# Kernel optimization log

Hardware: AMD Instinct MI355X
Metric: run time of the kernel (lower is better)

Reference implementation:

```python
import jax, jax.numpy as jnp
import numpy as np

B, L, V, D, H = 4096, 32, 50000, 300, 6
HD = D // H  # 50


def setup_inputs() -> dict:
    key = jax.random.key(0)
    ks = jax.random.split(key, 9)
    s = 0.02
    return {
        "title": jax.random.randint(ks[0], (B, L), 0, V),
        "emb": jax.random.normal(ks[1], (V, D), dtype=jnp.float32) * s,
        "pos_emb": jax.random.normal(ks[2], (512, D), dtype=jnp.float32) * s,
        "Wq": jax.random.normal(ks[3], (D, D), dtype=jnp.float32) * s,
        "bq": jnp.zeros((D,), jnp.float32),
        "Wk": jax.random.normal(ks[4], (D, D), dtype=jnp.float32) * s,
        "bk": jnp.zeros((D,), jnp.float32),
        "Wv": jax.random.normal(ks[5], (D, D), dtype=jnp.float32) * s,
        "bv": jnp.zeros((D,), jnp.float32),
        "Wo": jax.random.normal(ks[6], (D, D), dtype=jnp.float32) * s,
        "bo": jnp.zeros((D,), jnp.float32),
        "Va": jax.random.normal(ks[7], (D, D), dtype=jnp.float32) * s,
        "ba": jnp.zeros((D,), jnp.float32),
        "qw": jax.random.normal(ks[8], (D, 1), dtype=jnp.float32) * s,
    }


def reference(title, emb, pos_emb, Wq, bq, Wk, bk, Wv, bv, Wo, bo, Va, ba, qw):
    b, l = title.shape
    # word embedding + positional embedding
    x = emb[title] + pos_emb[:l][None, :, :]  # [B, L, D]

    def heads(y):  # [B, L, D] -> [B, H, L, HD]
        return y.reshape(b, l, H, HD).transpose(0, 2, 1, 3)

    # manual multi-head self-attention (mask is all-ones -> no masking effect)
    q = heads(x @ Wq.T + bq) / jnp.sqrt(jnp.float32(HD))
    k = heads(x @ Wk.T + bk)
    v = heads(x @ Wv.T + bv)
    scores = jnp.einsum("bhqd,bhkd->bhqk", q, k)  # [B, H, L, L]
    w = jax.nn.softmax(scores, axis=-1)  # dropout is identity in eval
    ctx = jnp.einsum("bhqk,bhkd->bhqd", w, v)
    ctx = ctx.transpose(0, 2, 1, 3).reshape(b, l, D)
    ctx = ctx @ Wo.T + bo  # [B, L, D]

    # additive attention pooling
    t = jnp.tanh(ctx @ Va.T + ba)          # [B, L, D]
    a = (t @ qw)[..., 0]                    # [B, L]
    alpha = jax.nn.softmax(a, axis=1)       # [B, L]
    out = jnp.einsum("bs,bsd->bd", alpha, ctx)  # [B, D]
    return out
```

## Files before the change

kernel.cpp:

```cpp
#include <hip/hip_runtime.h>
#include <math.h>

typedef _Float16 f16;
typedef _Float16 half8 __attribute__((ext_vector_type(8)));
typedef _Float16 half4 __attribute__((ext_vector_type(4)));
typedef float float4v __attribute__((ext_vector_type(4)));
typedef int int4v __attribute__((ext_vector_type(4)));

#define MFMA16(a, b, c) __builtin_amdgcn_mfma_f32_16x16x32_f16((a), (b), (c), 0, 0, 0)


#define WQKV_OFF 0u
#define BQKV_OFF 655360u
#define WO_OFF   659456u
#define WVA_OFF  864256u
#define BVA_OFF  1069056u
#define CBAR_OFF 1070336u
#define XF_OFF   3691776u

__device__ __forceinline__ float fast_tanh(float x) {
    float e = __expf(2.f * x);
    return 1.f - 2.f / (e + 1.f);
}

__global__ void repack1(const float* __restrict__ Wq, const float* __restrict__ Wk,
                        const float* __restrict__ Wv, const float* __restrict__ Wo,
                        const float* __restrict__ bq, const float* __restrict__ bk,
                        const float* __restrict__ bv,
                        f16* __restrict__ wqkvF, f16* __restrict__ wo16F,
                        float* __restrict__ bqkv) {
    int idx = blockIdx.x * 256 + threadIdx.x;
    const float rs = 0.14142135623730951f;
    if (idx < 327680) {
        int ntile = idx / 5120, rem = idx - ntile * 5120;
        int ks = rem / 512, r2 = rem - ks * 512;
        int lane = r2 >> 3, j = r2 & 7;
        int n = ntile * 16 + (lane & 15);
        int k = ks * 32 + (lane >> 4) * 8 + j;
        int g = n / 320, r = n - g * 320;
        float v = 0.f;
        if (r < 300 && k < 300) {
            if (g == 0) v = Wq[r * 300 + k] * rs;
            else if (g == 1) v = Wk[r * 300 + k];
            else if (g == 2) v = Wv[r * 300 + k];
        }
        wqkvF[idx] = (f16)v;
    } else if (idx < 430080) {
        int t = idx - 327680;
        int ntile = t / 5120, rem = t - ntile * 5120;
        int ks = rem / 512, r2 = rem - ks * 512;
        int lane = r2 >> 3, j = r2 & 7;
        int n = ntile * 16 + (lane & 15);
        int k = ks * 32 + (lane >> 4) * 8 + j;
        wo16F[t] = (f16)((n < 300 && k < 300) ? Wo[n * 300 + k] : 0.f);
    } else if (idx < 431104) {
        int n = idx - 430080;
        int g = n / 320, r = n - g * 320;
        float v = 0.f;
        if (r < 300) {
            if (g == 0) v = bq[r] * rs;
            else if (g == 1) v = bk[r];
            else if (g == 2) v = bv[r];
        }
        bqkv[n] = v;
    }
}

__global__ void repack2(const float* __restrict__ Va, const float* __restrict__ Wo,
                        f16* __restrict__ wvaF) {
    int bt = blockIdx.x;
    int mt = bt / 20, nt = bt % 20;
    int lane = threadIdx.x & 63;
    int lr = lane & 15, quad = lane >> 4;
    float4v acc = {0.f, 0.f, 0.f, 0.f};
    int m = mt * 16 + lr;
    int nn = nt * 16 + lr;
    for (int ks = 0; ks < 10; ++ks) {
        int c = ks * 32 + quad * 8;
        half8 af, bf;
#pragma unroll
        for (int j = 0; j < 8; ++j) {
            int cc = c + j;
            af[j] = (f16)((m < 300 && cc < 300) ? Va[m * 300 + cc] : 0.f);
            bf[j] = (f16)((nn < 300 && cc < 300) ? Wo[cc * 300 + nn] : 0.f);
        }
        acc = MFMA16(af, bf, acc);
    }
#pragma unroll
    for (int r = 0; r < 4; ++r) {
        int row = mt * 16 + quad * 4 + r;
        int col = nt * 16 + lr;
        int addr = ((row >> 4) * 10 + (col >> 5)) * 512 +
                   (((col >> 3) & 3) * 16 + (row & 15)) * 8 + (col & 7);
        wvaF[addr] = (f16)acc[r];
    }
}

__global__ void repack3(const float* __restrict__ Va, const float* __restrict__ bo,
                        const float* __restrict__ ba, float* __restrict__ bva) {
    int j = threadIdx.x;
    float s = 0.f;
    if (j < 300) {
        for (int k = 0; k < 300; ++k) s += Va[j * 300 + k] * bo[k];
        s += ba[j];
    }
    bva[j] = s;
}

__global__ void gather_kernel(const int* __restrict__ title, const float* __restrict__ emb,
                              const float* __restrict__ pos, f16* __restrict__ xF) {
    int c = blockIdx.x * 256 + threadIdx.x;
    int fragblk = c >> 6, lane = c & 63;
    int item = fragblk / 20, rem = fragblk - item * 20;
    int mt = rem / 10, ks = rem - mt * 10;
    int lr = lane & 15, quad = lane >> 4;
    int row = item * 32 + mt * 16 + lr;
    int col = ks * 32 + quad * 8;
    int t = title[row];
    int l = row & 31;
    half8 h;
    if (col + 8 <= 300) {
        float4v e0 = *(const float4v*)&emb[t * 300 + col];
        float4v e1 = *(const float4v*)&emb[t * 300 + col + 4];
        float4v p0 = *(const float4v*)&pos[l * 300 + col];
        float4v p1 = *(const float4v*)&pos[l * 300 + col + 4];
#pragma unroll
        for (int j = 0; j < 4; ++j) { h[j] = (f16)(e0[j] + p0[j]); h[4 + j] = (f16)(e1[j] + p1[j]); }
    } else {
#pragma unroll
        for (int j = 0; j < 8; ++j) {
            int cc = col + j;
            h[j] = (f16)((cc < 300) ? emb[t * 300 + cc] + pos[l * 300 + cc] : 0.f);
        }
    }
    *(half8*)&xF[c * 8] = h;
}

__global__ __launch_bounds__(512, 4) void qkvattn_kernel(
    const f16* __restrict__ xF, const f16* __restrict__ wqkvF,
    const float* __restrict__ bqkv, const f16* __restrict__ wvaF,
    const float* __restrict__ bva, const float* __restrict__ qw,
    f16* __restrict__ cbar) {
    __shared__ __align__(16) f16 qL[6 * 32 * 72];
    __shared__ __align__(16) f16 kL[6 * 32 * 72];
    __shared__ __align__(16) f16 vT[6 * 64 * 32];
    __shared__ float aL[32];
    const int ib = blockIdx.x, tid = threadIdx.x;
    const int w = tid >> 6, lane = tid & 63, lr = lane & 15, quad = lane >> 4;
    const float4v vz = {0.f, 0.f, 0.f, 0.f};
    const int4v z4 = {0, 0, 0, 0};

    for (int i = tid; i < 1344; i += 512) {
        int hrow = i / 7, c = i - hrow * 7;
        ((int*)&qL[hrow * 72 + 50])[c] = 0;
        ((int*)&kL[hrow * 72 + 50])[c] = 0;
    }
    for (int i = tid; i < 336; i += 512) {
        int t = i >> 2, c4 = i & 3;
        int h = t / 14, d = 50 + (t - (t / 14) * 14);
        ((int4v*)&vT[(h * 64 + d) * 32])[c4] = z4;
    }
    if (tid < 32) aL[tid] = 0.f;

    {
        float bb[8];
#pragma unroll
        for (int j = 0; j < 8; ++j) bb[j] = bqkv[(w * 8 + j) * 16 + lr];
        float4v acc[2][8];
#pragma unroll
        for (int mt = 0; mt < 2; ++mt)
#pragma unroll
            for (int j = 0; j < 8; ++j) acc[mt][j] = vz;
#pragma unroll
        for (int ks = 0; ks < 10; ++ks) {
            half8 a0 = *(const half8*)&xF[(((ib * 2 + 0) * 10 + ks) * 64 + lane) * 8];
            half8 a1 = *(const half8*)&xF[(((ib * 2 + 1) * 10 + ks) * 64 + lane) * 8];
#pragma unroll
            for (int j = 0; j < 8; ++j) {
                int tile = w * 8 + j;
                if (tile < 60) {
                    half8 bf = *(const half8*)&wqkvF[((tile * 10 + ks) * 64 + lane) * 8];
                    acc[0][j] = MFMA16(a0, bf, acc[0][j]);
                    acc[1][j] = MFMA16(a1, bf, acc[1][j]);
                }
            }
        }
#pragma unroll
        for (int j = 0; j < 8; ++j) {
            int tile = w * 8 + j;
            int wi = tile / 20;
            int n = tile * 16 + lr;
            int cc = n - wi * 320;
            if (wi < 3 && cc < 300) {
                int h = cc / 50, d = cc - h * 50;
                if (wi == 2) {
#pragma unroll
                    for (int mt = 0; mt < 2; ++mt) {
                        int row0 = mt * 16 + quad * 4;
                        half4 pk;
#pragma unroll
                        for (int r = 0; r < 4; ++r) pk[r] = (f16)(acc[mt][j][r] + bb[j]);
                        int idx = (h * 64 + d) * 32 + row0;
                        int byt = (idx * 2) ^ (((d >> 2) & 3) << 4);
                        *(half4*)((char*)vT + byt) = pk;
                    }
                } else {
                    f16* dst = (wi == 0) ? qL : kL;
#pragma unroll
                    for (int mt = 0; mt < 2; ++mt)
#pragma unroll
                        for (int r = 0; r < 4; ++r) {
                            int row = mt * 16 + quad * 4 + r;
                            dst[(h * 32 + row) * 72 + d] = (f16)(acc[mt][j][r] + bb[j]);
                        }
                }
            }
        }
    }
    __syncthreads();

    const int hh = w;
    if (w < 6) {
        float4v s00 = vz, s01 = vz, s10 = vz, s11 = vz;
#pragma unroll
        for (int ks = 0; ks < 2; ++ks) {
            int c = ks * 32 + quad * 8;
            half8 aq0 = *(const half8*)&qL[(hh * 32 + lr) * 72 + c];
            half8 aq1 = *(const half8*)&qL[(hh * 32 + 16 + lr) * 72 + c];
            half8 bk0 = *(const half8*)&kL[(hh * 32 + lr) * 72 + c];
            half8 bk1 = *(const half8*)&kL[(hh * 32 + 16 + lr) * 72 + c];
            s00 = MFMA16(aq0, bk0, s00);
            s01 = MFMA16(aq0, bk1, s01);
            s10 = MFMA16(aq1, bk0, s10);
            s11 = MFMA16(aq1, bk1, s11);
        }
        f16* ph = qL + hh * 32 * 72;
#pragma unroll
        for (int mt = 0; mt < 2; ++mt) {
            float4v sv0 = mt ? s10 : s00;
            float4v sv1 = mt ? s11 : s01;
#pragma unroll
            for (int r = 0; r < 4; ++r) {
                float v0 = sv0[r], v1 = sv1[r];
                float m = fmaxf(v0, v1);
#pragma unroll
                for (int off = 1; off < 16; off <<= 1) m = fmaxf(m, __shfl_xor(m, off, 64));
                float e0 = __expf(v0 - m), e1 = __expf(v1 - m);
                float ss = e0 + e1;
#pragma unroll
                for (int off = 1; off < 16; off <<= 1) ss += __shfl_xor(ss, off, 64);
                float inv = 1.0f / ss;
                int row = mt * 16 + quad * 4 + r;
                ph[row * 40 + lr] = (f16)(e0 * inv);
                ph[row * 40 + 16 + lr] = (f16)(e1 * inv);
            }
        }
    }
    __syncthreads();

    f16* scratch = kL;
    for (int i = tid; i < 32 * 28; i += 512) {
        int row = i / 28, cc = 300 + (i - row * 28);
        scratch[row * 328 + cc] = (f16)0.f;
    }
    if (w < 6) {
        int h = hh;
        f16* ph = qL + hh * 32 * 72;
        half8 aw0 = *(const half8*)&ph[lr * 40 + quad * 8];
        half8 aw1 = *(const half8*)&ph[(16 + lr) * 40 + quad * 8];
        float4v c0[4], c1[4];
#pragma unroll
        for (int nt = 0; nt < 4; ++nt) { c0[nt] = vz; c1[nt] = vz; }
#pragma unroll
        for (int nt = 0; nt < 4; ++nt) {
            int rIdx = nt * 16 + lr;
            int idx = (hh * 64 + rIdx) * 32 + quad * 8;
            int byt = (idx * 2) ^ (((rIdx >> 2) & 3) << 4);
            half8 bvf = *(const half8*)((const char*)vT + byt);
            c0[nt] = MFMA16(aw0, bvf, c0[nt]);
            c1[nt] = MFMA16(aw1, bvf, c1[nt]);
        }
#pragma unroll
        for (int mt = 0; mt < 2; ++mt)
#pragma unroll
            for (int nt = 0; nt < 4; ++nt)
#pragma unroll
                for (int r = 0; r < 4; ++r) {
                    int d = nt * 16 + lr;
                    if (d < 50) {
                        int row = mt * 16 + quad * 4 + r;
                        float4v cv = mt ? c1[nt] : c0[nt];
                        scratch[row * 328 + h * 50 + d] = (f16)cv[r];
                    }
                }
    }

    const int mtile = w >> 2, nsub = w & 3;
    half8 pbf[5];
    float pbva[5], pqw[5];
#pragma unroll
    for (int i = 0; i < 5; ++i) {
        int n = (nsub * 5 + i) * 16 + lr;
        pbf[i] = *(const half8*)&wvaF[(((nsub * 5 + i) * 10) * 64 + lane) * 8];
        pbva[i] = bva[n];
        pqw[i] = (n < 300) ? qw[n] : 0.f;
    }
    __syncthreads();

    {
        float4v vacc[5];
#pragma unroll
        for (int i = 0; i < 5; ++i) vacc[i] = vz;
        const int arow = (mtile * 16 + lr) * 328;
        {
            half8 a = *(const half8*)&scratch[arow + quad * 8];
#pragma unroll
            for (int i = 0; i < 5; ++i) vacc[i] = MFMA16(a, pbf[i], vacc[i]);
        }
#pragma unroll
        for (int ks = 1; ks < 10; ++ks) {
            half8 a = *(const half8*)&scratch[arow + ks * 32 + quad * 8];
#pragma unroll
            for (int i = 0; i < 5; ++i) {
                half8 bf = *(const half8*)&wvaF[((((nsub * 5 + i) * 10) + ks) * 64 + lane) * 8];
                vacc[i] = MFMA16(a, bf, vacc[i]);
            }
        }
        float ps[4] = {0.f, 0.f, 0.f, 0.f};
#pragma unroll
        for (int i = 0; i < 5; ++i) {
#pragma unroll
            for (int r = 0; r < 4; ++r) ps[r] += fast_tanh(vacc[i][r] + pbva[i]) * pqw[i];
        }
#pragma unroll
        for (int r = 0; r < 4; ++r)
#pragma unroll
            for (int off = 1; off < 16; off <<= 1) ps[r] += __shfl_xor(ps[r], off, 64);
        if (lr == 0) {
#pragma unroll
            for (int r = 0; r < 4; ++r) atomicAdd(&aL[mtile * 16 + quad * 4 + r], ps[r]);
        }
    }
    __syncthreads();

    {
        float av = aL[lane & 31];
        float m5 = av;
#pragma unroll
        for (int off = 1; off < 32; off <<= 1) m5 = fmaxf(m5, __shfl_xor(m5, off, 32));
        float e5 = __expf(av - m5);
        float ss5 = e5;
#pragma unroll
        for (int off = 1; off < 32; off <<= 1) ss5 += __shfl_xor(ss5, off, 32);
        float al = e5 / ss5;
        if (tid < 320) {
            int d = tid;
            float acc = 0.f;
#pragma unroll
            for (int l = 0; l < 32; ++l)
                acc += __shfl(al, l, 32) * (float)scratch[l * 328 + d];
            cbar[ib * 320 + d] = (f16)acc;
        }
    }
}

__global__ __launch_bounds__(512) void out_kernel(
    const f16* __restrict__ cbar, const f16* __restrict__ wo16F,
    const float* __restrict__ bo, float* __restrict__ out) {
    __shared__ __align__(16) f16 cA[32 * 328];
    const int mb = blockIdx.x, tid = threadIdx.x;
    const int w = tid >> 6, lane = tid & 63, lr = lane & 15, quad = lane >> 4;
    const int mh = w >> 2, nsub = w & 3;
    for (int i = tid; i < 1280; i += 512) {
        int row = i / 40, g = i - row * 40;
        *(half8*)&cA[row * 328 + g * 8] = *(const half8*)&cbar[(mb * 32 + row) * 320 + g * 8];
    }
    __syncthreads();
    const float4v vz = {0.f, 0.f, 0.f, 0.f};
    float4v acc[5];
#pragma unroll
    for (int i = 0; i < 5; ++i) acc[i] = vz;
#pragma unroll
    for (int ks = 0; ks < 10; ++ks) {
        half8 a = *(const half8*)&cA[(mh * 16 + lr) * 328 + ks * 32 + quad * 8];
#pragma unroll
        for (int i = 0; i < 5; ++i) {
            half8 bf = *(const half8*)&wo16F[((((nsub * 5 + i) * 10) + ks) * 64 + lane) * 8];
            acc[i] = MFMA16(a, bf, acc[i]);
        }
    }
#pragma unroll
    for (int i = 0; i < 5; ++i) {
        int n = (nsub * 5 + i) * 16 + lr;
        if (n < 300) {
            float bb = bo[n];
#pragma unroll
            for (int r = 0; r < 4; ++r)
                out[(mb * 32 + mh * 16 + quad * 4 + r) * 300 + n] = acc[i][r] + bb;
        }
    }
}

extern "C" void kernel_launch(void* const* d_in, const int* in_sizes, int n_in,
                              void* d_out, int out_size, void* d_ws, size_t ws_size,
                              hipStream_t stream) {
    const int* title = (const int*)d_in[0];
    const float* emb = (const float*)d_in[1];
    const float* pos = (const float*)d_in[2];
    const float* Wq = (const float*)d_in[3];
    const float* bq = (const float*)d_in[4];
    const float* Wk = (const float*)d_in[5];
    const float* bk = (const float*)d_in[6];
    const float* Wv = (const float*)d_in[7];
    const float* bv = (const float*)d_in[8];
    const float* Wo = (const float*)d_in[9];
    const float* bo = (const float*)d_in[10];
    const float* Va = (const float*)d_in[11];
    const float* ba = (const float*)d_in[12];
    const float* qw = (const float*)d_in[13];
    char* ws = (char*)d_ws;
    float* out = (float*)d_out;

    f16* wqkvF = (f16*)(ws + WQKV_OFF);
    float* bqkv = (float*)(ws + BQKV_OFF);
    f16* wo16F = (f16*)(ws + WO_OFF);
    f16* wvaF = (f16*)(ws + WVA_OFF);
    float* bva = (float*)(ws + BVA_OFF);
    f16* cbar = (f16*)(ws + CBAR_OFF);
    f16* xF = (f16*)(ws + XF_OFF);

    repack1<<<1684, 256, 0, stream>>>(Wq, Wk, Wv, Wo, bq, bk, bv, wqkvF, wo16F, bqkv);
    repack2<<<400, 64, 0, stream>>>(Va, Wo, wvaF);
    repack3<<<1, 320, 0, stream>>>(Va, bo, ba, bva);
    gather_kernel<<<20480, 256, 0, stream>>>(title, emb, pos, xF);
    qkvattn_kernel<<<4096, 512, 0, stream>>>(xF, wqkvF, bqkv, wvaF, bva, qw, cbar);
    out_kernel<<<128, 512, 0, stream>>>(cbar, wo16F, bo, out);
}
```

Baseline: 446.4 us.

## Fuse embedding gather into attention kernel and parallelize bias fold

The standalone gather kernel, which wrote the f16 embedding+position fragments to a global buffer, is removed. Each attention block now gathers its own 32 rows straight into shared memory, reusing the vT buffer before V is written, and runs the QKV MFMAs from LDS. This drops a global round trip of the activations and one launch, at the cost of an extra block barrier and exposed gather latency inside the main kernel. The single-block bias precompute is also spread over 320 wavefronts with a shuffle reduction.

```diff
diff --git a/kernel.cpp b/kernel.cpp
--- a/kernel.cpp
+++ b/kernel.cpp
@@ -16,7 +16,6 @@
 #define WVA_OFF  864256u
 #define BVA_OFF  1069056u
 #define CBAR_OFF 1070336u
-#define XF_OFF   3691776u
 
 __device__ __forceinline__ float fast_tanh(float x) {
     float e = __expf(2.f * x);
@@ -98,49 +97,23 @@
 
 __global__ void repack3(const float* __restrict__ Va, const float* __restrict__ bo,
                         const float* __restrict__ ba, float* __restrict__ bva) {
-    int j = threadIdx.x;
+    int j = blockIdx.x;
+    int lane = threadIdx.x;
     float s = 0.f;
     if (j < 300) {
-        for (int k = 0; k < 300; ++k) s += Va[j * 300 + k] * bo[k];
-        s += ba[j];
-    }
-    bva[j] = s;
-}
-
-__global__ void gather_kernel(const int* __restrict__ title, const float* __restrict__ emb,
-                              const float* __restrict__ pos, f16* __restrict__ xF) {
-    int c = blockIdx.x * 256 + threadIdx.x;
-    int fragblk = c >> 6, lane = c & 63;
-    int item = fragblk / 20, rem = fragblk - item * 20;
-    int mt = rem / 10, ks = rem - mt * 10;
-    int lr = lane & 15, quad = lane >> 4;
-    int row = item * 32 + mt * 16 + lr;
-    int col = ks * 32 + quad * 8;
-    int t = title[row];
-    int l = row & 31;
-    half8 h;
-    if (col + 8 <= 300) {
-        float4v e0 = *(const float4v*)&emb[t * 300 + col];
-        float4v e1 = *(const float4v*)&emb[t * 300 + col + 4];
-        float4v p0 = *(const float4v*)&pos[l * 300 + col];
-        float4v p1 = *(const float4v*)&pos[l * 300 + col + 4];
-#pragma unroll
-        for (int j = 0; j < 4; ++j) { h[j] = (f16)(e0[j] + p0[j]); h[4 + j] = (f16)(e1[j] + p1[j]); }
-    } else {
-#pragma unroll
-        for (int j = 0; j < 8; ++j) {
-            int cc = col + j;
-            h[j] = (f16)((cc < 300) ? emb[t * 300 + cc] + pos[l * 300 + cc] : 0.f);
-        }
-    }
-    *(half8*)&xF[c * 8] = h;
+        for (int k = lane; k < 300; k += 64) s += Va[j * 300 + k] * bo[k];
+    }
+#pragma unroll
+    for (int off = 1; off < 64; off <<= 1) s += __shfl_xor(s, off, 64);
+    if (lane == 0) bva[j] = (j < 300) ? s + ba[j] : 0.f;
 }
 
 __global__ __launch_bounds__(512, 4) void qkvattn_kernel(
-    const f16* __restrict__ xF, const f16* __restrict__ wqkvF,
-    const float* __restrict__ bqkv, const f16* __restrict__ wvaF,
-    const float* __restrict__ bva, const float* __restrict__ qw,
-    f16* __restrict__ cbar) {
+    const int* __restrict__ title, const float* __restrict__ emb,
+    const float* __restrict__ pos,
+    const f16* __restrict__ wqkvF, const float* __restrict__ bqkv,
+    const f16* __restrict__ wvaF, const float* __restrict__ bva,
+    const float* __restrict__ qw, f16* __restrict__ cbar) {
     __shared__ __align__(16) f16 qL[6 * 32 * 72];
     __shared__ __align__(16) f16 kL[6 * 32 * 72];
     __shared__ __align__(16) f16 vT[6 * 64 * 32];
@@ -149,71 +122,99 @@
     const int w = tid >> 6, lane = tid & 63, lr = lane & 15, quad = lane >> 4;
     const float4v vz = {0.f, 0.f, 0.f, 0.f};
     const int4v z4 = {0, 0, 0, 0};
-
+    f16* xA = vT;
+
+    for (int u = tid; u < 1280; u += 512) {
+        int fragblk = u >> 6, lu = u & 63;
+        int mt = fragblk / 10, ks = fragblk - mt * 10;
+        int row = mt * 16 + (lu & 15);
+        int col = ks * 32 + (lu >> 4) * 8;
+        int t = title[ib * 32 + row];
+        half8 h;
+        if (col + 8 <= 300) {
+            float4v e0 = *(const float4v*)&emb[t * 300 + col];
+            float4v e1 = *(const float4v*)&emb[t * 300 + col + 4];
+            float4v p0 = *(const float4v*)&pos[row * 300 + col];
+            float4v p1 = *(const float4v*)&pos[row * 300 + col + 4];
+#pragma unroll
+            for (int j = 0; j < 4; ++j) {
+                h[j] = (f16)(e0[j] + p0[j]);
+                h[4 + j] = (f16)(e1[j] + p1[j]);
+            }
+        } else {
+#pragma unroll
+            for (int j = 0; j < 8; ++j) {
+                int cc = col + j;
+                h[j] = (f16)((cc < 300) ? emb[t * 300 + cc] + pos[row * 300 + cc] : 0.f);
+            }
+        }
+        *(half8*)&xA[u * 8] = h;
+    }
     for (int i = tid; i < 1344; i += 512) {
         int hrow = i / 7, c = i - hrow * 7;
         ((int*)&qL[hrow * 72 + 50])[c] = 0;
         ((int*)&kL[hrow * 72 + 50])[c] = 0;
     }
+    if (tid < 32) aL[tid] = 0.f;
+    float bb[8];
+#pragma unroll
+    for (int j = 0; j < 8; ++j) bb[j] = bqkv[(w * 8 + j) * 16 + lr];
+    __syncthreads();
+
+    float4v acc[2][8];
+#pragma unroll
+    for (int mt = 0; mt < 2; ++mt)
+#pragma unroll
+        for (int j = 0; j < 8; ++j) acc[mt][j] = vz;
+#pragma unroll
+    for (int ks = 0; ks < 10; ++ks) {
+        half8 a0 = *(const half8*)&xA[(ks * 64 + lane) * 8];
+        half8 a1 = *(const half8*)&xA[((10 + ks) * 64 + lane) * 8];
+#pragma unroll
+        for (int j = 0; j < 8; ++j) {
+            int tile = w * 8 + j;
+            if (tile < 60) {
+                half8 bf = *(const half8*)&wqkvF[((tile * 10 + ks) * 64 + lane) * 8];
+                acc[0][j] = MFMA16(a0, bf, acc[0][j]);
+                acc[1][j] = MFMA16(a1, bf, acc[1][j]);
+            }
+        }
+    }
+    __syncthreads();
+
     for (int i = tid; i < 336; i += 512) {
         int t = i >> 2, c4 = i & 3;
         int h = t / 14, d = 50 + (t - (t / 14) * 14);
         ((int4v*)&vT[(h * 64 + d) * 32])[c4] = z4;
     }
-    if (tid < 32) aL[tid] = 0.f;
-
-    {
-        float bb[8];
-#pragma unroll
-        for (int j = 0; j < 8; ++j) bb[j] = bqkv[(w * 8 + j) * 16 + lr];
-        float4v acc[2][8];
-#pragma unroll
-        for (int mt = 0; mt < 2; ++mt)
-#pragma unroll
-            for (int j = 0; j < 8; ++j) acc[mt][j] = vz;
-#pragma unroll
-        for (int ks = 0; ks < 10; ++ks) {
-            half8 a0 = *(const half8*)&xF[(((ib * 2 + 0) * 10 + ks) * 64 + lane) * 8];
-            half8 a1 = *(const half8*)&xF[(((ib * 2 + 1) * 10 + ks) * 64 + lane) * 8];
-#pragma unroll
-            for (int j = 0; j < 8; ++j) {
-                int tile = w * 8 + j;
-                if (tile < 60) {
-                    half8 bf = *(const half8*)&wqkvF[((tile * 10 + ks) * 64 + lane) * 8];
-                    acc[0][j] = MFMA16(a0, bf, acc[0][j]);
-                    acc[1][j] = MFMA16(a1, bf, acc[1][j]);
+#pragma unroll
+    for (int j = 0; j < 8; ++j) {
+        int tile = w * 8 + j;
+        int wi = tile / 20;
+        int n = tile * 16 + lr;
+        int cc = n - wi * 320;
+        if (wi < 3 && cc < 300) {
+            int h = cc / 50, d = cc - h * 50;
+            if (wi == 2) {
+#pragma unroll
+                for (int mt = 0; mt < 2; ++mt) {
+                    int row0 = mt * 16 + quad * 4;
+                    half4 pk;
+#pragma unroll
+                    for (int r = 0; r < 4; ++r) pk[r] = (f16)(acc[mt][j][r] + bb[j]);
+                    int idx = (h * 64 + d) * 32 + row0;
+                    int byt = (idx * 2) ^ (((d >> 2) & 3) << 4);
+                    *(half4*)((char*)vT + byt) = pk;
                 }
-            }
-        }
-#pragma unroll
-        for (int j = 0; j < 8; ++j) {
-            int tile = w * 8 + j;
-            int wi = tile / 20;
-            int n = tile * 16 + lr;
-            int cc = n - wi * 320;
-            if (wi < 3 && cc < 300) {
-                int h = cc / 50, d = cc - h * 50;
-                if (wi == 2) {
-#pragma unroll
-                    for (int mt = 0; mt < 2; ++mt) {
-                        int row0 = mt * 16 + quad * 4;
-                        half4 pk;
-#pragma unroll
-                        for (int r = 0; r < 4; ++r) pk[r] = (f16)(acc[mt][j][r] + bb[j]);
-                        int idx = (h * 64 + d) * 32 + row0;
-                        int byt = (idx * 2) ^ (((d >> 2) & 3) << 4);
-                        *(half4*)((char*)vT + byt) = pk;
+            } else {
+                f16* dst = (wi == 0) ? qL : kL;
+#pragma unroll
+                for (int mt = 0; mt < 2; ++mt)
+#pragma unroll
+                    for (int r = 0; r < 4; ++r) {
+                        int row = mt * 16 + quad * 4 + r;
+                        dst[(h * 32 + row) * 72 + d] = (f16)(acc[mt][j][r] + bb[j]);
                     }
-                } else {
-                    f16* dst = (wi == 0) ? qL : kL;
-#pragma unroll
-                    for (int mt = 0; mt < 2; ++mt)
-#pragma unroll
-                        for (int r = 0; r < 4; ++r) {
-                            int row = mt * 16 + quad * 4 + r;
-                            dst[(h * 32 + row) * 72 + d] = (f16)(acc[mt][j][r] + bb[j]);
-                        }
-                }
             }
         }
     }
@@ -355,11 +356,11 @@
         float al = e5 / ss5;
         if (tid < 320) {
             int d = tid;
-            float acc = 0.f;
+            float acc6 = 0.f;
 #pragma unroll
             for (int l = 0; l < 32; ++l)
-                acc += __shfl(al, l, 32) * (float)scratch[l * 328 + d];
-            cbar[ib * 320 + d] = (f16)acc;
+                acc6 += __shfl(al, l, 32) * (float)scratch[l * 328 + d];
+            cbar[ib * 320 + d] = (f16)acc6;
         }
     }
 }
@@ -427,12 +428,10 @@
     f16* wvaF = (f16*)(ws + WVA_OFF);
     float* bva = (float*)(ws + BVA_OFF);
     f16* cbar = (f16*)(ws + CBAR_OFF);
-    f16* xF = (f16*)(ws + XF_OFF);
 
     repack1<<<1684, 256, 0, stream>>>(Wq, Wk, Wv, Wo, bq, bk, bv, wqkvF, wo16F, bqkv);
     repack2<<<400, 64, 0, stream>>>(Va, Wo, wvaF);
-    repack3<<<1, 320, 0, stream>>>(Va, bo, ba, bva);
-    gather_kernel<<<20480, 256, 0, stream>>>(title, emb, pos, xF);
-    qkvattn_kernel<<<4096, 512, 0, stream>>>(xF, wqkvF, bqkv, wvaF, bva, qw, cbar);
+    repack3<<<320, 64, 0, stream>>>(Va, bo, ba, bva);
+    qkvattn_kernel<<<4096, 512, 0, stream>>>(title, emb, pos, wqkvF, bqkv, wvaF, bva, qw, cbar);
     out_kernel<<<128, 512, 0, stream>>>(cbar, wo16F, bo, out);
 }
```

Result: faster. 431.2 us (-3.4%).
